# Optimization experiments

Measured on AMD Instinct MI355X. Metric: run time of the kernel, lower is better.

## Reference

```python
import jax, jax.numpy as jnp
import numpy as np


def setup_inputs() -> dict:
    key = jax.random.key(0)
    B, T = 16, 2048
    # encoding dim must be T + 1 (1 padding row + T signal rows)
    x = jax.random.normal(key, (B, T + 1, T), dtype=jnp.float32)
    return {"x": x}


def reference(x):
    # x: [B, D, T] with D == T + 1
    B, D, T = x.shape
    pad = x[:, 0, :]                 # [B, T]  (index_select dim=1, idx [0])
    sig = x[:, 1:T + 1, :]           # [B, T, T] (index_select dim=1, idx 1..T)
    # L1 norm over encoding dim (torch.norm(signal, dim=1, p=1))
    sig_norm = jnp.sum(jnp.abs(sig), axis=1)          # [B, T]
    # 2-way softmax over (pad, norm); first column == sigmoid(pad - norm)
    w = jax.nn.sigmoid(pad - sig_norm)                # [B, T]
    pad_weighted = (w * pad)[:, None, :]              # [B, 1, T]
    # NB: torch reshapes signal to [B*T, T] row-major, so the (1 - w) gate
    # indexed by flat row i = (b, d) multiplies along the *encoding* axis.
    sig_weighted = (1.0 - w)[:, :, None] * sig        # [B, T, T]
    return jnp.concatenate([pad_weighted, sig_weighted], axis=1)  # [B, T+1, T]
```

## Files before the change

kernel.cpp:

```cpp
#include <hip/hip_runtime.h>


#define TDIM 2048
#define BDIM 16
#define ROWS 32
#define NTHREADS 512

typedef float floatx4 __attribute__((ext_vector_type(4)));

__global__ __launch_bounds__(NTHREADS, 8) void colsum_kernel(const float* __restrict__ x,
                                                             float* __restrict__ ws) {
    const int blk  = blockIdx.x;
    const int b    = blk / (TDIM / ROWS);
    const int tile = blk % (TDIM / ROWS);
    const int r0   = tile * ROWS;
    const int t    = threadIdx.x;

    const size_t plane = (size_t)(TDIM + 1) * TDIM;
    const float* sig = x + (size_t)b * plane + TDIM;
    const float* base = sig + (size_t)r0 * TDIM + 4 * t;

    float a0 = 0.f, a1 = 0.f, a2 = 0.f, a3 = 0.f;
    #pragma unroll 8
    for (int r = 0; r < ROWS; ++r) {
        const floatx4 v = *reinterpret_cast<const floatx4*>(base + (size_t)r * TDIM);
        a0 += fabsf(v.x); a1 += fabsf(v.y); a2 += fabsf(v.z); a3 += fabsf(v.w);
    }

    float* wsb = ws + (size_t)b * TDIM + 4 * t;
    atomicAdd(wsb + 0, a0);
    atomicAdd(wsb + 1, a1);
    atomicAdd(wsb + 2, a2);
    atomicAdd(wsb + 3, a3);
}

__global__ __launch_bounds__(NTHREADS, 8) void scale_kernel(const float* __restrict__ x,
                                                            const float* __restrict__ ws,
                                                            float* __restrict__ out) {
    const int nb   = BDIM * (TDIM / ROWS);
    const int blk  = nb - 1 - blockIdx.x;
    const int b    = blk / (TDIM / ROWS);
    const int tile = blk % (TDIM / ROWS);
    const int r0   = tile * ROWS;
    const int t    = threadIdx.x;

    const size_t plane = (size_t)(TDIM + 1) * TDIM;
    const float* xb  = x   + (size_t)b * plane;
    float*       ob  = out + (size_t)b * plane;
    const float* sig = xb + TDIM;

    __shared__ float lds_scale[ROWS];
    if (t < ROWS) {
        const float s = ws[(size_t)b * TDIM + r0 + t];
        const float p = xb[r0 + t];
        const float w = 1.0f / (1.0f + expf(s - p));
        ob[r0 + t]    = w * p;
        lds_scale[t]  = 1.0f - w;
    }
    __syncthreads();

    const float* srcb = sig + (size_t)r0 * TDIM;
    float*       dstb = ob + TDIM + (size_t)r0 * TDIM;
    #pragma unroll 4
    for (int r = 0; r < ROWS; ++r) {
        floatx4 v = *reinterpret_cast<const floatx4*>(srcb + (size_t)r * TDIM + 4 * t);
        const float sc = lds_scale[r];
        v.x *= sc; v.y *= sc; v.z *= sc; v.w *= sc;
        __builtin_nontemporal_store(v, reinterpret_cast<floatx4*>(dstb + (size_t)r * TDIM + 4 * t));
    }
}

extern "C" void kernel_launch(void* const* d_in, const int* in_sizes, int n_in,
                              void* d_out, int out_size, void* d_ws, size_t ws_size,
                              hipStream_t stream) {
    const float* x   = (const float*)d_in[0];
    float*       out = (float*)d_out;
    float*       ws  = (float*)d_ws;

    hipMemsetAsync(ws, 0, (size_t)BDIM * TDIM * sizeof(float), stream);

    const int nblocks = BDIM * (TDIM / ROWS);
    colsum_kernel<<<nblocks, NTHREADS, 0, stream>>>(x, ws);
    scale_kernel <<<nblocks, NTHREADS, 0, stream>>>(x, ws, out);
}
```

Measured before the change: 147.9 us.

## Replace atomic column-sum accumulation with per-block partials reduced in scale kernel

Each colsum block now writes its 2048-element partial column sum to a private workspace slice instead of issuing atomicAdds into a shared per-batch buffer. The scale kernel reduces the 64 partials for its 32 rows through shared memory before computing the sigmoid gate. This removes the hipMemsetAsync and the atomic contention, at the cost of a larger workspace (64x) and extra reads in the scale kernel. The second kernel now reads the partials in a strided pattern, which may be poorly coalesced.

```diff
diff --git a/kernel.cpp b/kernel.cpp
--- a/kernel.cpp
+++ b/kernel.cpp
@@ -5,55 +5,61 @@
 #define BDIM 16
 #define ROWS 32
 #define NTHREADS 512
+#define NBLK (BDIM * (TDIM / ROWS))
 
 typedef float floatx4 __attribute__((ext_vector_type(4)));
 
 __global__ __launch_bounds__(NTHREADS, 8) void colsum_kernel(const float* __restrict__ x,
                                                              float* __restrict__ ws) {
-    const int blk  = blockIdx.x;
-    const int b    = blk / (TDIM / ROWS);
-    const int tile = blk % (TDIM / ROWS);
-    const int r0   = tile * ROWS;
-    const int t    = threadIdx.x;
+    const int k  = blockIdx.x;
+    const int b  = k >> 6;
+    const int r0 = (k & 63) * ROWS;
+    const int t  = threadIdx.x;
 
     const size_t plane = (size_t)(TDIM + 1) * TDIM;
-    const float* sig = x + (size_t)b * plane + TDIM;
-    const float* base = sig + (size_t)r0 * TDIM + 4 * t;
+    const float* src = x + (size_t)b * plane + TDIM + (size_t)r0 * TDIM + 4 * t;
 
     float a0 = 0.f, a1 = 0.f, a2 = 0.f, a3 = 0.f;
     #pragma unroll 8
     for (int r = 0; r < ROWS; ++r) {
-        const floatx4 v = *reinterpret_cast<const floatx4*>(base + (size_t)r * TDIM);
+        const floatx4 v = *reinterpret_cast<const floatx4*>(src + (size_t)r * TDIM);
         a0 += fabsf(v.x); a1 += fabsf(v.y); a2 += fabsf(v.z); a3 += fabsf(v.w);
     }
 
-    float* wsb = ws + (size_t)b * TDIM + 4 * t;
-    atomicAdd(wsb + 0, a0);
-    atomicAdd(wsb + 1, a1);
-    atomicAdd(wsb + 2, a2);
-    atomicAdd(wsb + 3, a3);
+    floatx4 p4; p4.x = a0; p4.y = a1; p4.z = a2; p4.w = a3;
+    *reinterpret_cast<floatx4*>(ws + (size_t)k * TDIM + 4 * t) = p4;
 }
 
 __global__ __launch_bounds__(NTHREADS, 8) void scale_kernel(const float* __restrict__ x,
                                                             const float* __restrict__ ws,
                                                             float* __restrict__ out) {
-    const int nb   = BDIM * (TDIM / ROWS);
-    const int blk  = nb - 1 - blockIdx.x;
-    const int b    = blk / (TDIM / ROWS);
-    const int tile = blk % (TDIM / ROWS);
-    const int r0   = tile * ROWS;
-    const int t    = threadIdx.x;
+    const int k  = NBLK - 1 - blockIdx.x;
+    const int b  = k >> 6;
+    const int r0 = (k & 63) * ROWS;
+    const int t  = threadIdx.x;
 
     const size_t plane = (size_t)(TDIM + 1) * TDIM;
     const float* xb  = x   + (size_t)b * plane;
     float*       ob  = out + (size_t)b * plane;
     const float* sig = xb + TDIM;
 
+    __shared__ float red[16][ROWS];
     __shared__ float lds_scale[ROWS];
+    const int c  = t & 31;
+    const int jg = t >> 5;
+    float s = 0.f;
+    #pragma unroll
+    for (int j = 0; j < 4; ++j)
+        s += ws[(size_t)(b * 64 + jg * 4 + j) * TDIM + r0 + c];
+    red[jg][c] = s;
+    __syncthreads();
+
     if (t < ROWS) {
-        const float s = ws[(size_t)b * TDIM + r0 + t];
+        float tot = 0.f;
+        #pragma unroll
+        for (int j = 0; j < 16; ++j) tot += red[j][t];
         const float p = xb[r0 + t];
-        const float w = 1.0f / (1.0f + expf(s - p));
+        const float w = 1.0f / (1.0f + expf(tot - p));
         ob[r0 + t]    = w * p;
         lds_scale[t]  = 1.0f - w;
     }
@@ -77,9 +83,6 @@
     float*       out = (float*)d_out;
     float*       ws  = (float*)d_ws;
 
-    hipMemsetAsync(ws, 0, (size_t)BDIM * TDIM * sizeof(float), stream);
-
-    const int nblocks = BDIM * (TDIM / ROWS);
-    colsum_kernel<<<nblocks, NTHREADS, 0, stream>>>(x, ws);
-    scale_kernel <<<nblocks, NTHREADS, 0, stream>>>(x, ws, out);
+    colsum_kernel<<<NBLK, NTHREADS, 0, stream>>>(x, ws);
+    scale_kernel <<<NBLK, NTHREADS, 0, stream>>>(x, ws, out);
 }
```

Measured after the change: 140.1 us. 5.2% less time.
